# Kernel optimization log

Hardware: AMD Instinct MI355X
Metric: run time of the kernel (lower is better)

## Reference

```python
import jax, jax.numpy as jnp
import numpy as np

CHANNELS = [(3, 64), (64, 64), (64, 128), (128, 128), (128, 256), (256, 256), (256, 256),
            (256, 512), (512, 512), (512, 512), (512, 512), (512, 512), (512, 512)]
HW = 256
IN_FEAT = 512 * (HW // 32) * (HW // 32)  # 32768


def _conv(x, w):
    # 3x3, stride 1, pad 1, NCHW / OIHW, no bias
    return jax.lax.conv_general_dilated(x, w, (1, 1), ((1, 1), (1, 1)),
                                         dimension_numbers=("NCHW", "OIHW", "NCHW"))


def _maxpool2(x):
    return jax.lax.reduce_window(x, -jnp.inf, jax.lax.max, (1, 1, 2, 2), (1, 1, 2, 2), "VALID")


def setup_inputs() -> dict:
    key = jax.random.key(0)
    keys = jax.random.split(key, 17)
    inp = {"x": jax.random.normal(keys[0], (1, 3, HW, HW), jnp.float32),
           "H": HW, "W": HW, "nTh": 32, "nTw": 32}
    for i, (cin, cout) in enumerate(CHANNELS):
        scale = (1.0 / np.sqrt(9.0 * cin)).astype(np.float32) if hasattr(np.sqrt(9.0 * cin), 'astype') else 1.0 / np.sqrt(9.0 * cin)
        inp[f"cw{i + 1}"] = jax.random.normal(keys[1 + i], (cout, cin, 3, 3), jnp.float32) * np.float32(1.0 / np.sqrt(9.0 * cin))
    inp["fw1"] = jax.random.normal(keys[14], (4096, IN_FEAT), jnp.float32) * np.float32(1.0 / np.sqrt(IN_FEAT))
    inp["fw2"] = jax.random.normal(keys[15], (4096, 4096), jnp.float32) * np.float32(1.0 / np.sqrt(4096))
    inp["fw3"] = jax.random.normal(keys[16], (1000, 4096), jnp.float32) * np.float32(1.0 / np.sqrt(4096))
    return inp


def reference(x, H, W, nTh, nTw, cw1, cw2, cw3, cw4, cw5, cw6, cw7, cw8, cw9, cw10,
              cw11, cw12, cw13, fw1, fw2, fw3):
    # VGG-16 conv stack; tiling in the original is an execution schedule only,
    # the math equals the untiled stack. conv -> relu repeated, maxpool per block.
    conv_ws = [cw1, cw2, cw3, cw4, cw5, cw6, cw7, cw8, cw9, cw10, cw11, cw12, cw13]
    blocks = [(0, 2), (2, 4), (4, 7), (7, 10), (10, 13)]
    h = x
    for lo, hi in blocks:
        for w in conv_ws[lo:hi]:
            h = jax.nn.relu(_conv(h, w))
        h = _maxpool2(h)
    h = h.reshape(h.shape[0], -1)          # [1, 32768]
    h = h @ fw1.T                           # fc1 (no bias, no relu, as in source)
    h = h @ fw2.T                           # fc2
    h = h @ fw3.T                           # fc3 -> [1, 1000]
    return h
```

## Files before the change

kernel.cpp:

```cpp
#include <hip/hip_runtime.h>
#include <cstddef>


typedef __attribute__((ext_vector_type(8))) short short8;
typedef __attribute__((ext_vector_type(4))) float f32x4;

__device__ inline unsigned short f2bf(float f) {
    unsigned int u = __builtin_bit_cast(unsigned int, f);
    u += 0x7FFF + ((u >> 16) & 1);
    return (unsigned short)(u >> 16);
}

__device__ __forceinline__ void gl_lds16(const void* src, unsigned m0v) {
    asm volatile("s_mov_b32 m0, %1\n\t"
                 "global_load_lds_dwordx4 %0, off"
                 :: "v"(src), "s"(m0v) : "memory");
}

struct WtDesc { const float* src; unsigned dst; int cin; int cout; int blk0; };
struct WtArgs { WtDesc d[12]; };

__global__ __launch_bounds__(256)
void wt_all_k(WtArgs A, unsigned short* __restrict__ wt, unsigned short* __restrict__ guard)
{
    __shared__ unsigned short lds[4][9 * 520];
    const int tid = threadIdx.x, wv = tid >> 6, lane = tid & 63;
    if (blockIdx.x == 0 && tid < 128) guard[tid] = 0;

    int l = 0;
#pragma unroll
    for (int i = 1; i < 12; ++i) l = ((int)blockIdx.x >= A.d[i].blk0) ? i : l;
    const WtDesc D = A.d[l];
    const int co = ((int)blockIdx.x - D.blk0) * 4 + wv;
    const int n = D.cin * 9;
    const int cinP = D.cin + 8;

    const float4* src = (const float4*)(D.src + (size_t)co * n);
    for (int i = lane; i < (n >> 2); i += 64) {
        float4 v = src[i];
        unsigned short b[4] = {f2bf(v.x), f2bf(v.y), f2bf(v.z), f2bf(v.w)};
        const int f0 = i * 4;
#pragma unroll
        for (int k = 0; k < 4; ++k) {
            const int f = f0 + k, ci = f / 9, pos = f - ci * 9;
            lds[wv][pos * cinP + ci] = b[k];
        }
    }
    __syncthreads();
    unsigned short* dstb = wt + D.dst;
#pragma unroll 1
    for (int pos = 0; pos < 9; ++pos) {
        unsigned short* drow = dstb + ((size_t)pos * D.cout + co) * D.cin;
        for (int c4 = lane; c4 < (D.cin >> 2); c4 += 64) {
            ushort4 u = *(const ushort4*)&lds[wv][pos * cinP + c4 * 4];
            *(ushort4*)(drow + c4 * 4) = u;
        }
    }
}

template<int PR, int CO, int MODE>
__global__ __launch_bounds__(256, 2)
void conv_mfma_k(const unsigned short* __restrict__ act,
                 const unsigned short* __restrict__ wt,
                 const unsigned short* __restrict__ guard,
                 void* __restrict__ outp,
                 int Cin, int Cout, int H, int W, int chunkCi)
{
    constexpr int NT = PR / 4;
    constexpr int MT = CO / 16;
    constexpr int ICELLS = (PR + 2) * 18;
    constexpr int ITASK = ICELLS * 4;
    constexpr int ITIN = (ITASK + 255) / 256;
    constexpr int IBYTES = ((ITASK + 63) & ~63) * 16;
    constexpr int WTASK = 9 * CO * 4;
    constexpr int WIT = (WTASK + 255) / 256;
    constexpr int WBYTES = 9 * CO * 64;
    constexpr int VL = WIT + ITIN;

    __shared__ __align__(16) unsigned short wLds[2 * WBYTES / 2];
    __shared__ __align__(16) unsigned short iLds[2 * IBYTES / 2];
    __shared__ __align__(16) unsigned short dump[512];

    const int tid = threadIdx.x;
    const int lane = tid & 63, wv = tid >> 6;
    const int half = lane >> 4, l15 = lane & 15;
    const int tilesX = W >> 4;
    const int pY = blockIdx.x / tilesX, pX = blockIdx.x - pY * tilesX;
    const int y0 = pY * PR, x0 = pX * 16;
    const int cob = blockIdx.y, s = blockIdx.z;
    const int ciBeg = s * chunkCi;
    const int nCh = chunkCi >> 5;

    f32x4 acc[MT][NT];
#pragma unroll
    for (int mt = 0; mt < MT; ++mt)
#pragma unroll
        for (int nt = 0; nt < NT; ++nt) acc[mt][nt] = (f32x4){0.f, 0.f, 0.f, 0.f};

    auto STAGE = [&](int buf, int ci0) {
        const unsigned wB = (unsigned)(size_t)wLds + buf * WBYTES;
        const unsigned iB = (unsigned)(size_t)iLds + buf * IBYTES;
        const unsigned dB = (unsigned)(size_t)dump;
#pragma unroll
        for (int it = 0; it < WIT; ++it) {
            const int idx = it * 256 + tid;
            const int cell = idx >> 2, q = idx & 3;
            const int pos = cell / CO, co = cell % CO;
            const bool real = idx < WTASK;
            const unsigned short* src = real ?
                wt + (size_t)(pos * Cout + cob * CO + co) * Cin + ci0 + q * 8 : guard;
            const bool eng = (it * 256 + wv * 64) < WTASK;
            gl_lds16(src, __builtin_amdgcn_readfirstlane(
                eng ? wB + (unsigned)(it * 4096 + wv * 1024) : dB));
        }
#pragma unroll
        for (int it = 0; it < ITIN; ++it) {
            const int idx = it * 256 + tid;
            const int cell = idx >> 2, q = idx & 3;
            const int r = cell / 18, c = cell - r * 18;
            const int y = y0 - 1 + r, x = x0 - 1 + c;
            const bool ok = (idx < ITASK) & (y >= 0) & (y < H) & (x >= 0) & (x < W);
            const unsigned short* src = ok ?
                act + (size_t)(y * W + x) * Cin + ci0 + q * 8 : guard;
            const bool eng = (it * 256 + wv * 64) < ITASK;
            gl_lds16(src, __builtin_amdgcn_readfirstlane(
                eng ? iB + (unsigned)(it * 4096 + wv * 1024) : dB));
        }
    };

    STAGE(0, ciBeg);
    for (int t = 0; t < nCh; ++t) {
        const int buf = t & 1;
        if (t + 1 < nCh) {
            STAGE(buf ^ 1, ciBeg + ((t + 1) << 5));
            if constexpr (VL == 8)  asm volatile("s_waitcnt vmcnt(8)" ::: "memory");
            else if constexpr (VL == 11) asm volatile("s_waitcnt vmcnt(11)" ::: "memory");
            else asm volatile("s_waitcnt vmcnt(0)" ::: "memory");
        } else {
            asm volatile("s_waitcnt vmcnt(0)" ::: "memory");
        }
        __builtin_amdgcn_s_barrier();
        asm volatile("" ::: "memory");

        const unsigned short* wP = wLds + buf * (WBYTES / 2);
        const unsigned short* iP = iLds + buf * (IBYTES / 2);
#pragma unroll
        for (int ky = 0; ky < 3; ++ky)
#pragma unroll
        for (int kx = 0; kx < 3; ++kx) {
            const int pos = ky * 3 + kx;
            short8 a[MT];
#pragma unroll
            for (int mt = 0; mt < MT; ++mt)
                a[mt] = *(const short8*)&wP[((pos * CO) + (mt << 4) + l15) * 32 + half * 8];
#pragma unroll
            for (int nt = 0; nt < NT; ++nt) {
                const short8 b = *(const short8*)
                    &iP[((wv * NT + nt + ky) * 18 + l15 + kx) * 32 + half * 8];
#pragma unroll
                for (int mt = 0; mt < MT; ++mt)
                    acc[mt][nt] = __builtin_amdgcn_mfma_f32_16x16x32_bf16(a[mt], b, acc[mt][nt], 0, 0, 0);
            }
        }
        asm volatile("" ::: "memory");
        __builtin_amdgcn_s_barrier();
    }

    const int xg = x0 + l15;
    if (MODE == 3) {
        const int Wo = W >> 1;
#pragma unroll
        for (int mt = 0; mt < MT; ++mt)
#pragma unroll
        for (int nt = 0; nt < NT; nt += 2) {
            f32x4 a;
#pragma unroll
            for (int j = 0; j < 4; ++j) a[j] = fmaxf(acc[mt][nt][j], acc[mt][nt + 1][j]);
            f32x4 m;
#pragma unroll
            for (int j = 0; j < 4; ++j) m[j] = fmaxf(a[j], __shfl_xor(a[j], 1, 64));
            if ((l15 & 1) == 0) {
                const int yo = (y0 + wv * NT + nt) >> 1;
                const int xo = xg >> 1;
                const int co = cob * CO + (mt << 4) + half * 4;
                ushort4 u;
                u.x = f2bf(fmaxf(m[0], 0.f));
                u.y = f2bf(fmaxf(m[1], 0.f));
                u.z = f2bf(fmaxf(m[2], 0.f));
                u.w = f2bf(fmaxf(m[3], 0.f));
                *(ushort4*)((unsigned short*)outp + ((size_t)(yo * Wo + xo) * Cout + co)) = u;
            }
        }
    } else {
#pragma unroll
        for (int mt = 0; mt < MT; ++mt)
#pragma unroll
        for (int nt = 0; nt < NT; ++nt) {
            const int yg = y0 + wv * NT + nt;
            const int co = cob * CO + (mt << 4) + half * 4;
            const size_t base = (size_t)(yg * W + xg) * Cout + co;
            if (MODE == 2) {
                float4 v = make_float4(acc[mt][nt][0], acc[mt][nt][1], acc[mt][nt][2], acc[mt][nt][3]);
                *(float4*)((float*)outp + (size_t)s * Cout * H * W + base) = v;
            } else {
                ushort4 u;
                u.x = f2bf(fmaxf(acc[mt][nt][0], 0.f));
                u.y = f2bf(fmaxf(acc[mt][nt][1], 0.f));
                u.z = f2bf(fmaxf(acc[mt][nt][2], 0.f));
                u.w = f2bf(fmaxf(acc[mt][nt][3], 0.f));
                *(ushort4*)((unsigned short*)outp + base) = u;
            }
        }
    }
}

#define TILE 16
#define COB  32
__global__ __launch_bounds__(256)
void conv1_k(const float* __restrict__ in, const float* __restrict__ wt,
             unsigned short* __restrict__ out)
{
    const int Cin = 3, H = 256, W = 256, HW = H * W;
    __shared__ float sIn[2][648];
    __shared__ float sWt[2][768];

    const int tid = threadIdx.x;
    const int bx = blockIdx.x, by = blockIdx.y, co_blk = blockIdx.z;
    const int co_grp = tid >> 6;
    const int lane = tid & 63;
    const int tx = lane & 7, ty = lane >> 3;
    const int x0 = bx * TILE, y0 = by * TILE;

    int iLdsI[3], iG[3], iSub[3]; bool iOk[3];
    int wLdsI[3], wG[3], wSub[3]; bool wOk[3];
#pragma unroll
    for (int j = 0; j < 3; ++j) {
        int i = tid + j * 256;
        iOk[j] = false; iLdsI[j] = 0; iG[j] = 0; iSub[j] = 0;
        if (i < 648) {
            int sub = i / 324; int r = i - sub * 324;
            int iy = r / 18;   int ix = r - iy * 18;
            iSub[j] = sub; iLdsI[j] = sub * 324 + r;
            int y = y0 - 1 + iy, x = x0 - 1 + ix;
            if (y >= 0 && y < H && x >= 0 && x < W) { iOk[j] = true; iG[j] = sub * HW + y * W + x; }
        }
        wOk[j] = false; wLdsI[j] = 0; wG[j] = 0; wSub[j] = 0;
        if (i < 576) {
            int sub = i / 288; int r = i - sub * 288;
            int col = r / 9;   int k = r - col * 9;
            wSub[j] = sub; wLdsI[j] = sub * 384 + col * 12 + k;
            wG[j] = ((co_blk * COB + col) * Cin + sub) * 9 + k;
            wOk[j] = true;
        }
    }

    float4 acc[8];
#pragma unroll
    for (int c = 0; c < 8; ++c) acc[c] = make_float4(0.f, 0.f, 0.f, 0.f);

    const int nSteps = 2;
    float rIn[3], rWt[3];
    {
#pragma unroll
        for (int j = 0; j < 3; ++j)
            rIn[j] = (iOk[j] && iSub[j] < 3) ? in[iG[j]] : 0.f;
#pragma unroll
        for (int j = 0; j < 3; ++j)
            rWt[j] = (wOk[j] && wSub[j] < 3) ? wt[wG[j]] : 0.f;
#pragma unroll
        for (int j = 0; j < 3; ++j) { if (tid + j * 256 < 648) sIn[0][iLdsI[j]] = rIn[j]; }
#pragma unroll
        for (int j = 0; j < 3; ++j) { if (tid + j * 256 < 576) sWt[0][wLdsI[j]] = rWt[j]; }
    }

    for (int t = 0; t < nSteps; ++t) {
        __syncthreads();
        const bool more = (t + 1) < nSteps;
        if (more) {
            const int ci0 = 2;
#pragma unroll
            for (int j = 0; j < 3; ++j)
                rIn[j] = (iOk[j] && (ci0 + iSub[j]) < 3) ? in[(size_t)ci0 * HW + iG[j]] : 0.f;
#pragma unroll
            for (int j = 0; j < 3; ++j)
                rWt[j] = (wOk[j] && (ci0 + wSub[j]) < 3) ? wt[(size_t)ci0 * 9 + wG[j]] : 0.f;
        }
        const int buf = t & 1;
        const float* sI = sIn[buf];
        const float* sW = sWt[buf];
#pragma unroll
        for (int sub = 0; sub < 2; ++sub) {
            float wv[4][4];
            const float* sp = sI + sub * 324 + (2 * ty) * 18 + 2 * tx;
#pragma unroll
            for (int r = 0; r < 4; ++r) {
                float2 a = *(const float2*)(sp + r * 18);
                float2 b = *(const float2*)(sp + r * 18 + 2);
                wv[r][0] = a.x; wv[r][1] = a.y; wv[r][2] = b.x; wv[r][3] = b.y;
            }
#pragma unroll
            for (int c = 0; c < 8; ++c) {
                const float* wp = sW + sub * 384 + (co_grp * 8 + c) * 12;
                float4 w0 = *(const float4*)wp;
                float4 w1 = *(const float4*)(wp + 4);
                float  w8 = wp[8];
                const float wk[9] = {w0.x, w0.y, w0.z, w0.w, w1.x, w1.y, w1.z, w1.w, w8};
                float* ac = (float*)&acc[c];
#pragma unroll
                for (int py = 0; py < 2; ++py)
#pragma unroll
                for (int px = 0; px < 2; ++px) {
                    float sacc = ac[py * 2 + px];
#pragma unroll
                    for (int kk = 0; kk < 9; ++kk)
                        sacc = fmaf(wv[py + kk / 3][px + kk % 3], wk[kk], sacc);
                    ac[py * 2 + px] = sacc;
                }
            }
        }
        if (more) {
#pragma unroll
            for (int j = 0; j < 3; ++j) { if (tid + j * 256 < 648) sIn[buf ^ 1][iLdsI[j]] = rIn[j]; }
#pragma unroll
            for (int j = 0; j < 3; ++j) { if (tid + j * 256 < 576) sWt[buf ^ 1][wLdsI[j]] = rWt[j]; }
        }
    }

    const int co0 = co_blk * COB + co_grp * 8;
#pragma unroll
    for (int py = 0; py < 2; ++py)
#pragma unroll
    for (int px = 0; px < 2; ++px) {
        const int y = y0 + 2 * ty + py, x = x0 + 2 * tx + px;
        unsigned short u8[8];
#pragma unroll
        for (int c = 0; c < 8; ++c)
            u8[c] = f2bf(fmaxf(((const float*)&acc[c])[py * 2 + px], 0.f));
        *(uint4*)(out + (size_t)(y * W + x) * 64 + co0) = *(uint4*)u8;
    }
}

__global__ __launch_bounds__(256)
void reduce_cvt_k(const float* __restrict__ P, unsigned short* __restrict__ out,
                  int n4, int S)
{
    int i = blockIdx.x * 256 + threadIdx.x;
    if (i >= n4) return;
    const float4* p4 = (const float4*)P;
    float4 a = p4[i];
    for (int s = 1; s < S; ++s) {
        float4 b = p4[(size_t)i + (size_t)s * n4];
        a.x += b.x; a.y += b.y; a.z += b.z; a.w += b.w;
    }
    ushort4 u;
    u.x = f2bf(fmaxf(a.x, 0.f)); u.y = f2bf(fmaxf(a.y, 0.f));
    u.z = f2bf(fmaxf(a.z, 0.f)); u.w = f2bf(fmaxf(a.w, 0.f));
    *(ushort4*)(out + (size_t)i * 4) = u;
}

__global__ __launch_bounds__(256)
void reduce_pool_cvt_k(const float* __restrict__ P, unsigned short* __restrict__ out,
                       int C, int H, int W, int S)
{
    const int C4 = C >> 2, Wo = W >> 1, Ho = H >> 1;
    const int n = Ho * Wo * C4;
    int i = blockIdx.x * 256 + threadIdx.x;
    if (i >= n) return;
    const int c4 = i % C4, p = i / C4;
    const int yo = p / Wo, xo = p - yo * Wo;
    const size_t CHW = (size_t)C * H * W;
    const size_t b = (size_t)(2 * yo * W + 2 * xo) * C + c4 * 4;
    float4 v[4] = {{0,0,0,0},{0,0,0,0},{0,0,0,0},{0,0,0,0}};
    for (int s = 0; s < S; ++s) {
        const float* ps = P + s * CHW;
        float4 t0 = *(const float4*)(ps + b);
        float4 t1 = *(const float4*)(ps + b + C);
        float4 t2 = *(const float4*)(ps + b + (size_t)W * C);
        float4 t3 = *(const float4*)(ps + b + (size_t)W * C + C);
        v[0].x += t0.x; v[0].y += t0.y; v[0].z += t0.z; v[0].w += t0.w;
        v[1].x += t1.x; v[1].y += t1.y; v[1].z += t1.z; v[1].w += t1.w;
        v[2].x += t2.x; v[2].y += t2.y; v[2].z += t2.z; v[2].w += t2.w;
        v[3].x += t3.x; v[3].y += t3.y; v[3].z += t3.z; v[3].w += t3.w;
    }
    ushort4 u;
    u.x = f2bf(fmaxf(fmaxf(fmaxf(v[0].x, v[1].x), fmaxf(v[2].x, v[3].x)), 0.f));
    u.y = f2bf(fmaxf(fmaxf(fmaxf(v[0].y, v[1].y), fmaxf(v[2].y, v[3].y)), 0.f));
    u.z = f2bf(fmaxf(fmaxf(fmaxf(v[0].z, v[1].z), fmaxf(v[2].z, v[3].z)), 0.f));
    u.w = f2bf(fmaxf(fmaxf(fmaxf(v[0].w, v[1].w), fmaxf(v[2].w, v[3].w)), 0.f));
    *(ushort4*)(out + (size_t)p * C + c4 * 4) = u;
}

__global__ __launch_bounds__(256)
void reduce_pool_f32_k(const float* __restrict__ P, float* __restrict__ out,
                       int C, int H, int W, int S)
{
    const int Wo = W >> 1, Ho = H >> 1;
    const int n = Ho * Wo * C;
    int i = blockIdx.x * 256 + threadIdx.x;
    if (i >= n) return;
    const int c = i % C, p = i / C;
    const int yo = p / Wo, xo = p - yo * Wo;
    const size_t CHW = (size_t)C * H * W;
    float v0 = 0.f, v1 = 0.f, v2 = 0.f, v3 = 0.f;
    const size_t b = (size_t)(2 * yo * W + 2 * xo) * C + c;
    for (int s = 0; s < S; ++s) {
        const float* ps = P + s * CHW;
        v0 += ps[b]; v1 += ps[b + C]; v2 += ps[b + (size_t)W * C]; v3 += ps[b + (size_t)W * C + C];
    }
    out[(size_t)c * (Ho * Wo) + p] = fmaxf(fmaxf(fmaxf(v0, v1), fmaxf(v2, v3)), 0.f);
}

__global__ __launch_bounds__(256)
void gemv_k(const float* __restrict__ Wm, const float* __restrict__ xv,
            float* __restrict__ y, int K)
{
    __shared__ float red[4];
    const int tid = threadIdx.x;
    const float4* row = (const float4*)(Wm + (size_t)blockIdx.x * K);
    const float4* x4  = (const float4*)xv;
    const int K4 = K >> 2;
    float sum = 0.f;
    for (int i = tid; i < K4; i += 256) {
        float4 a = row[i], b = x4[i];
        sum += a.x * b.x + a.y * b.y + a.z * b.z + a.w * b.w;
    }
#pragma unroll
    for (int off = 32; off > 0; off >>= 1) sum += __shfl_down(sum, off, 64);
    if ((tid & 63) == 0) red[tid >> 6] = sum;
    __syncthreads();
    if (tid == 0) y[blockIdx.x] = red[0] + red[1] + red[2] + red[3];
}

extern "C" void kernel_launch(void* const* d_in, const int* in_sizes, int n_in,
                              void* d_out, int out_size, void* d_ws, size_t ws_size,
                              hipStream_t stream)
{
    (void)in_sizes; (void)n_in; (void)out_size; (void)ws_size;
    const float* x = (const float*)d_in[0];
    const float* cw[13];
    for (int i = 0; i < 13; ++i) cw[i] = (const float*)d_in[5 + i];
    const float* fw1 = (const float*)d_in[18];
    const float* fw2 = (const float*)d_in[19];
    const float* fw3 = (const float*)d_in[20];
    float* outp = (float*)d_out;

    static const int CIN[12]  = {64, 64, 128, 128, 256, 256, 256, 512, 512, 512, 512, 512};
    static const int COUT[12] = {64, 128, 128, 256, 256, 256, 512, 512, 512, 512, 512, 512};

    char* ws = (char*)d_ws;
    size_t wOff[12]; size_t o = 0;
    for (int i = 0; i < 12; ++i) { wOff[i] = o; o += (size_t)9 * COUT[i] * CIN[i]; }
    unsigned short* WT = (unsigned short*)ws;
    unsigned short* guardp = WT + o;
    size_t ao = ((o + 128) * 2 + 255) & ~(size_t)255;
    unsigned short* bA = (unsigned short*)(ws + ao);
    unsigned short* bB = (unsigned short*)(ws + ao + 8388608);
    char* Pr = ws + ao + 2 * 8388608;
    float* Pf = (float*)Pr;
    float* fcIn = (float*)bA;
    float* F1 = (float*)bB;
    float* F2 = F1 + 4096;

    WtArgs wa; int blk = 0;
    {
        size_t oo = 0;
        for (int i = 0; i < 12; ++i) {
            wa.d[i].src = cw[i + 1];
            wa.d[i].dst = (unsigned)oo;
            wa.d[i].cin = CIN[i];
            wa.d[i].cout = COUT[i];
            wa.d[i].blk0 = blk;
            oo += (size_t)9 * COUT[i] * CIN[i];
            blk += COUT[i] / 4;
        }
    }
    wt_all_k<<<blk, 256, 0, stream>>>(wa, WT, guardp);

    conv1_k<<<dim3(16, 16, 2), 256, 0, stream>>>(x, cw[0], bA);

    conv_mfma_k<16, 32, 3><<<dim3(256, 2, 1), 256, 0, stream>>>(bA, WT + wOff[0], guardp, bB, 64, 64, 256, 256, 64);
    conv_mfma_k<8, 32, 0><<<dim3(128, 4, 1), 256, 0, stream>>>(bB, WT + wOff[1], guardp, bA, 64, 128, 128, 128, 64);
    conv_mfma_k<8, 32, 3><<<dim3(128, 4, 1), 256, 0, stream>>>(bA, WT + wOff[2], guardp, bB, 128, 128, 128, 128, 128);
    conv_mfma_k<8, 32, 2><<<dim3(32, 8, 2), 256, 0, stream>>>(bB, WT + wOff[3], guardp, Pf, 128, 256, 64, 64, 64);
    reduce_cvt_k<<<(262144 + 255) / 256, 256, 0, stream>>>(Pf, bA, 262144, 2);
    conv_mfma_k<8, 32, 2><<<dim3(32, 8, 2), 256, 0, stream>>>(bA, WT + wOff[4], guardp, Pf, 256, 256, 64, 64, 128);
    reduce_cvt_k<<<(262144 + 255) / 256, 256, 0, stream>>>(Pf, bB, 262144, 2);
    conv_mfma_k<8, 32, 2><<<dim3(32, 8, 2), 256, 0, stream>>>(bB, WT + wOff[5], guardp, Pf, 256, 256, 64, 64, 128);
    reduce_pool_cvt_k<<<(65536 + 255) / 256, 256, 0, stream>>>(Pf, bA, 256, 64, 64, 2);
    conv_mfma_k<8, 32, 2><<<dim3(8, 16, 4), 256, 0, stream>>>(bA, WT + wOff[6], guardp, Pf, 256, 512, 32, 32, 64);
    reduce_cvt_k<<<(131072 + 255) / 256, 256, 0, stream>>>(Pf, bB, 131072, 4);
    conv_mfma_k<8, 32, 2><<<dim3(8, 16, 4), 256, 0, stream>>>(bB, WT + wOff[7], guardp, Pf, 512, 512, 32, 32, 128);
    reduce_cvt_k<<<(131072 + 255) / 256, 256, 0, stream>>>(Pf, bA, 131072, 4);
    conv_mfma_k<8, 32, 2><<<dim3(8, 16, 4), 256, 0, stream>>>(bA, WT + wOff[8], guardp, Pf, 512, 512, 32, 32, 128);
    reduce_pool_cvt_k<<<(32768 + 255) / 256, 256, 0, stream>>>(Pf, bB, 512, 32, 32, 4);
    conv_mfma_k<8, 32, 2><<<dim3(2, 16, 16), 256, 0, stream>>>(bB, WT + wOff[9], guardp, Pf, 512, 512, 16, 16, 32);
    reduce_cvt_k<<<(32768 + 255) / 256, 256, 0, stream>>>(Pf, bA, 32768, 16);
    conv_mfma_k<8, 32, 2><<<dim3(2, 16, 16), 256, 0, stream>>>(bA, WT + wOff[10], guardp, Pf, 512, 512, 16, 16, 32);
    reduce_cvt_k<<<(32768 + 255) / 256, 256, 0, stream>>>(Pf, bB, 32768, 16);
    conv_mfma_k<8, 32, 2><<<dim3(2, 16, 16), 256, 0, stream>>>(bB, WT + wOff[11], guardp, Pf, 512, 512, 16, 16, 32);
    reduce_pool_f32_k<<<(32768 + 255) / 256, 256, 0, stream>>>(Pf, fcIn, 512, 16, 16, 16);

    gemv_k<<<4096, 256, 0, stream>>>(fw1, fcIn, F1, 32768);
    gemv_k<<<4096, 256, 0, stream>>>(fw2, F1, F2, 4096);
    gemv_k<<<1000, 256, 0, stream>>>(fw3, F2, outp, 4096);
}
```

Before: 968.7 us.

## Drop split-K partials and fuse ReLU/pool into conv epilogues

Removes the split-K path from the MFMA conv kernel, so each block now loops over the full input-channel range. ReLU, bf16 conversion and 2x2 max-pool are applied in the conv epilogue, and the last layer writes fp32 NCHW straight into the FC input. This eliminates the separate reduce and reduce-pool kernels and the fp32 partial-sum round trips through memory. To keep some parallelism, the 32x32 and 16x16 layers switch to 4-row tiles. Those deep layers still launch far fewer blocks, each running a longer K loop, which risks underfilling the GPU.

```diff
diff --git a/kernel.cpp b/kernel.cpp
--- a/kernel.cpp
+++ b/kernel.cpp
@@ -64,9 +64,9 @@
                  const unsigned short* __restrict__ wt,
                  const unsigned short* __restrict__ guard,
                  void* __restrict__ outp,
-                 int Cin, int Cout, int H, int W, int chunkCi)
+                 int Cin, int Cout, int H, int W)
 {
-    constexpr int NT = PR / 4;
+    constexpr int NT = (PR + 3) / 4;
     constexpr int MT = CO / 16;
     constexpr int ICELLS = (PR + 2) * 18;
     constexpr int ITASK = ICELLS * 4;
@@ -76,6 +76,8 @@
     constexpr int WIT = (WTASK + 255) / 256;
     constexpr int WBYTES = 9 * CO * 64;
     constexpr int VL = WIT + ITIN;
+    static_assert(VL == 7 || VL == 8 || VL == 11, "unexpected stage depth");
+    static_assert(MODE == 0 || ((MODE == 3 || MODE == 4) && (NT % 2) == 0), "pool needs even NT");
 
     __shared__ __align__(16) unsigned short wLds[2 * WBYTES / 2];
     __shared__ __align__(16) unsigned short iLds[2 * IBYTES / 2];
@@ -87,9 +89,8 @@
     const int tilesX = W >> 4;
     const int pY = blockIdx.x / tilesX, pX = blockIdx.x - pY * tilesX;
     const int y0 = pY * PR, x0 = pX * 16;
-    const int cob = blockIdx.y, s = blockIdx.z;
-    const int ciBeg = s * chunkCi;
-    const int nCh = chunkCi >> 5;
+    const int cob = blockIdx.y;
+    const int nCh = Cin >> 5;
 
     f32x4 acc[MT][NT];
 #pragma unroll
@@ -128,14 +129,14 @@
         }
     };
 
-    STAGE(0, ciBeg);
+    STAGE(0, 0);
     for (int t = 0; t < nCh; ++t) {
         const int buf = t & 1;
         if (t + 1 < nCh) {
-            STAGE(buf ^ 1, ciBeg + ((t + 1) << 5));
-            if constexpr (VL == 8)  asm volatile("s_waitcnt vmcnt(8)" ::: "memory");
-            else if constexpr (VL == 11) asm volatile("s_waitcnt vmcnt(11)" ::: "memory");
-            else asm volatile("s_waitcnt vmcnt(0)" ::: "memory");
+            STAGE(buf ^ 1, (t + 1) << 5);
+            if constexpr (VL == 7)  asm volatile("s_waitcnt vmcnt(7)" ::: "memory");
+            else if constexpr (VL == 8)  asm volatile("s_waitcnt vmcnt(8)" ::: "memory");
+            else asm volatile("s_waitcnt vmcnt(11)" ::: "memory");
         } else {
             asm volatile("s_waitcnt vmcnt(0)" ::: "memory");
         }
@@ -167,7 +168,7 @@
     }
 
     const int xg = x0 + l15;
-    if (MODE == 3) {
+    if constexpr (MODE == 3 || MODE == 4) {
         const int Wo = W >> 1;
 #pragma unroll
         for (int mt = 0; mt < MT; ++mt)
@@ -183,12 +184,21 @@
                 const int yo = (y0 + wv * NT + nt) >> 1;
                 const int xo = xg >> 1;
                 const int co = cob * CO + (mt << 4) + half * 4;
-                ushort4 u;
-                u.x = f2bf(fmaxf(m[0], 0.f));
-                u.y = f2bf(fmaxf(m[1], 0.f));
-                u.z = f2bf(fmaxf(m[2], 0.f));
-                u.w = f2bf(fmaxf(m[3], 0.f));
-                *(ushort4*)((unsigned short*)outp + ((size_t)(yo * Wo + xo) * Cout + co)) = u;
+                if constexpr (MODE == 3) {
+                    ushort4 u;
+                    u.x = f2bf(fmaxf(m[0], 0.f));
+                    u.y = f2bf(fmaxf(m[1], 0.f));
+                    u.z = f2bf(fmaxf(m[2], 0.f));
+                    u.w = f2bf(fmaxf(m[3], 0.f));
+                    *(ushort4*)((unsigned short*)outp + ((size_t)(yo * Wo + xo) * Cout + co)) = u;
+                } else {
+                    const int Ho = W >> 1;  (void)Ho;
+                    float* op = (float*)outp;
+                    const int hw = (W >> 1) * (W >> 1);
+#pragma unroll
+                    for (int j = 0; j < 4; ++j)
+                        op[(size_t)(co + j) * hw + yo * Wo + xo] = fmaxf(m[j], 0.f);
+                }
             }
         }
     } else {
@@ -199,17 +209,12 @@
             const int yg = y0 + wv * NT + nt;
             const int co = cob * CO + (mt << 4) + half * 4;
             const size_t base = (size_t)(yg * W + xg) * Cout + co;
-            if (MODE == 2) {
-                float4 v = make_float4(acc[mt][nt][0], acc[mt][nt][1], acc[mt][nt][2], acc[mt][nt][3]);
-                *(float4*)((float*)outp + (size_t)s * Cout * H * W + base) = v;
-            } else {
-                ushort4 u;
-                u.x = f2bf(fmaxf(acc[mt][nt][0], 0.f));
-                u.y = f2bf(fmaxf(acc[mt][nt][1], 0.f));
-                u.z = f2bf(fmaxf(acc[mt][nt][2], 0.f));
-                u.w = f2bf(fmaxf(acc[mt][nt][3], 0.f));
-                *(ushort4*)((unsigned short*)outp + base) = u;
-            }
+            ushort4 u;
+            u.x = f2bf(fmaxf(acc[mt][nt][0], 0.f));
+            u.y = f2bf(fmaxf(acc[mt][nt][1], 0.f));
+            u.z = f2bf(fmaxf(acc[mt][nt][2], 0.f));
+            u.w = f2bf(fmaxf(acc[mt][nt][3], 0.f));
+            *(ushort4*)((unsigned short*)outp + base) = u;
         }
     }
 }
@@ -338,76 +343,6 @@
             u8[c] = f2bf(fmaxf(((const float*)&acc[c])[py * 2 + px], 0.f));
         *(uint4*)(out + (size_t)(y * W + x) * 64 + co0) = *(uint4*)u8;
     }
-}
-
-__global__ __launch_bounds__(256)
-void reduce_cvt_k(const float* __restrict__ P, unsigned short* __restrict__ out,
-                  int n4, int S)
-{
-    int i = blockIdx.x * 256 + threadIdx.x;
-    if (i >= n4) return;
-    const float4* p4 = (const float4*)P;
-    float4 a = p4[i];
-    for (int s = 1; s < S; ++s) {
-        float4 b = p4[(size_t)i + (size_t)s * n4];
-        a.x += b.x; a.y += b.y; a.z += b.z; a.w += b.w;
-    }
-    ushort4 u;
-    u.x = f2bf(fmaxf(a.x, 0.f)); u.y = f2bf(fmaxf(a.y, 0.f));
-    u.z = f2bf(fmaxf(a.z, 0.f)); u.w = f2bf(fmaxf(a.w, 0.f));
-    *(ushort4*)(out + (size_t)i * 4) = u;
-}
-
-__global__ __launch_bounds__(256)
-void reduce_pool_cvt_k(const float* __restrict__ P, unsigned short* __restrict__ out,
-                       int C, int H, int W, int S)
-{
-    const int C4 = C >> 2, Wo = W >> 1, Ho = H >> 1;
-    const int n = Ho * Wo * C4;
-    int i = blockIdx.x * 256 + threadIdx.x;
-    if (i >= n) return;
-    const int c4 = i % C4, p = i / C4;
-    const int yo = p / Wo, xo = p - yo * Wo;
-    const size_t CHW = (size_t)C * H * W;
-    const size_t b = (size_t)(2 * yo * W + 2 * xo) * C + c4 * 4;
-    float4 v[4] = {{0,0,0,0},{0,0,0,0},{0,0,0,0},{0,0,0,0}};
-    for (int s = 0; s < S; ++s) {
-        const float* ps = P + s * CHW;
-        float4 t0 = *(const float4*)(ps + b);
-        float4 t1 = *(const float4*)(ps + b + C);
-        float4 t2 = *(const float4*)(ps + b + (size_t)W * C);
-        float4 t3 = *(const float4*)(ps + b + (size_t)W * C + C);
-        v[0].x += t0.x; v[0].y += t0.y; v[0].z += t0.z; v[0].w += t0.w;
-        v[1].x += t1.x; v[1].y += t1.y; v[1].z += t1.z; v[1].w += t1.w;
-        v[2].x += t2.x; v[2].y += t2.y; v[2].z += t2.z; v[2].w += t2.w;
-        v[3].x += t3.x; v[3].y += t3.y; v[3].z += t3.z; v[3].w += t3.w;
-    }
-    ushort4 u;
-    u.x = f2bf(fmaxf(fmaxf(fmaxf(v[0].x, v[1].x), fmaxf(v[2].x, v[3].x)), 0.f));
-    u.y = f2bf(fmaxf(fmaxf(fmaxf(v[0].y, v[1].y), fmaxf(v[2].y, v[3].y)), 0.f));
-    u.z = f2bf(fmaxf(fmaxf(fmaxf(v[0].z, v[1].z), fmaxf(v[2].z, v[3].z)), 0.f));
-    u.w = f2bf(fmaxf(fmaxf(fmaxf(v[0].w, v[1].w), fmaxf(v[2].w, v[3].w)), 0.f));
-    *(ushort4*)(out + (size_t)p * C + c4 * 4) = u;
-}
-
-__global__ __launch_bounds__(256)
-void reduce_pool_f32_k(const float* __restrict__ P, float* __restrict__ out,
-                       int C, int H, int W, int S)
-{
-    const int Wo = W >> 1, Ho = H >> 1;
-    const int n = Ho * Wo * C;
-    int i = blockIdx.x * 256 + threadIdx.x;
-    if (i >= n) return;
-    const int c = i % C, p = i / C;
-    const int yo = p / Wo, xo = p - yo * Wo;
-    const size_t CHW = (size_t)C * H * W;
-    float v0 = 0.f, v1 = 0.f, v2 = 0.f, v3 = 0.f;
-    const size_t b = (size_t)(2 * yo * W + 2 * xo) * C + c;
-    for (int s = 0; s < S; ++s) {
-        const float* ps = P + s * CHW;
-        v0 += ps[b]; v1 += ps[b + C]; v2 += ps[b + (size_t)W * C]; v3 += ps[b + (size_t)W * C + C];
-    }
-    out[(size_t)c * (Ho * Wo) + p] = fmaxf(fmaxf(fmaxf(v0, v1), fmaxf(v2, v3)), 0.f);
 }
 
 __global__ __launch_bounds__(256)
@@ -455,8 +390,6 @@
     size_t ao = ((o + 128) * 2 + 255) & ~(size_t)255;
     unsigned short* bA = (unsigned short*)(ws + ao);
     unsigned short* bB = (unsigned short*)(ws + ao + 8388608);
-    char* Pr = ws + ao + 2 * 8388608;
-    float* Pf = (float*)Pr;
     float* fcIn = (float*)bA;
     float* F1 = (float*)bB;
     float* F2 = F1 + 4096;
@@ -478,27 +411,18 @@
 
     conv1_k<<<dim3(16, 16, 2), 256, 0, stream>>>(x, cw[0], bA);
 
-    conv_mfma_k<16, 32, 3><<<dim3(256, 2, 1), 256, 0, stream>>>(bA, WT + wOff[0], guardp, bB, 64, 64, 256, 256, 64);
-    conv_mfma_k<8, 32, 0><<<dim3(128, 4, 1), 256, 0, stream>>>(bB, WT + wOff[1], guardp, bA, 64, 128, 128, 128, 64);
-    conv_mfma_k<8, 32, 3><<<dim3(128, 4, 1), 256, 0, stream>>>(bA, WT + wOff[2], guardp, bB, 128, 128, 128, 128, 128);
-    conv_mfma_k<8, 32, 2><<<dim3(32, 8, 2), 256, 0, stream>>>(bB, WT + wOff[3], guardp, Pf, 128, 256, 64, 64, 64);
-    reduce_cvt_k<<<(262144 + 255) / 256, 256, 0, stream>>>(Pf, bA, 262144, 2);
-    conv_mfma_k<8, 32, 2><<<dim3(32, 8, 2), 256, 0, stream>>>(bA, WT + wOff[4], guardp, Pf, 256, 256, 64, 64, 128);
-    reduce_cvt_k<<<(262144 + 255) / 256, 256, 0, stream>>>(Pf, bB, 262144, 2);
-    conv_mfma_k<8, 32, 2><<<dim3(32, 8, 2), 256, 0, stream>>>(bB, WT + wOff[5], guardp, Pf, 256, 256, 64, 64, 128);
-    reduce_pool_cvt_k<<<(65536 + 255) / 256, 256, 0, stream>>>(Pf, bA, 256, 64, 64, 2);
-    conv_mfma_k<8, 32, 2><<<dim3(8, 16, 4), 256, 0, stream>>>(bA, WT + wOff[6], guardp, Pf, 256, 512, 32, 32, 64);
-    reduce_cvt_k<<<(131072 + 255) / 256, 256, 0, stream>>>(Pf, bB, 131072, 4);
-    conv_mfma_k<8, 32, 2><<<dim3(8, 16, 4), 256, 0, stream>>>(bB, WT + wOff[7], guardp, Pf, 512, 512, 32, 32, 128);
-    reduce_cvt_k<<<(131072 + 255) / 256, 256, 0, stream>>>(Pf, bA, 131072, 4);
-    conv_mfma_k<8, 32, 2><<<dim3(8, 16, 4), 256, 0, stream>>>(bA, WT + wOff[8], guardp, Pf, 512, 512, 32, 32, 128);
-    reduce_pool_cvt_k<<<(32768 + 255) / 256, 256, 0, stream>>>(Pf, bB, 512, 32, 32, 4);
-    conv_mfma_k<8, 32, 2><<<dim3(2, 16, 16), 256, 0, stream>>>(bB, WT + wOff[9], guardp, Pf, 512, 512, 16, 16, 32);
-    reduce_cvt_k<<<(32768 + 255) / 256, 256, 0, stream>>>(Pf, bA, 32768, 16);
-    conv_mfma_k<8, 32, 2><<<dim3(2, 16, 16), 256, 0, stream>>>(bA, WT + wOff[10], guardp, Pf, 512, 512, 16, 16, 32);
-    reduce_cvt_k<<<(32768 + 255) / 256, 256, 0, stream>>>(Pf, bB, 32768, 16);
-    conv_mfma_k<8, 32, 2><<<dim3(2, 16, 16), 256, 0, stream>>>(bB, WT + wOff[11], guardp, Pf, 512, 512, 16, 16, 32);
-    reduce_pool_f32_k<<<(32768 + 255) / 256, 256, 0, stream>>>(Pf, fcIn, 512, 16, 16, 16);
+    conv_mfma_k<16, 32, 3><<<dim3(256, 2), 256, 0, stream>>>(bA, WT + wOff[0], guardp, bB, 64, 64, 256, 256);
+    conv_mfma_k<8, 32, 0><<<dim3(128, 4), 256, 0, stream>>>(bB, WT + wOff[1], guardp, bA, 64, 128, 128, 128);
+    conv_mfma_k<8, 32, 3><<<dim3(128, 4), 256, 0, stream>>>(bA, WT + wOff[2], guardp, bB, 128, 128, 128, 128);
+    conv_mfma_k<8, 32, 0><<<dim3(32, 8), 256, 0, stream>>>(bB, WT + wOff[3], guardp, bA, 128, 256, 64, 64);
+    conv_mfma_k<8, 32, 0><<<dim3(32, 8), 256, 0, stream>>>(bA, WT + wOff[4], guardp, bB, 256, 256, 64, 64);
+    conv_mfma_k<8, 32, 3><<<dim3(32, 8), 256, 0, stream>>>(bB, WT + wOff[5], guardp, bA, 256, 256, 64, 64);
+    conv_mfma_k<4, 32, 0><<<dim3(16, 16), 256, 0, stream>>>(bA, WT + wOff[6], guardp, bB, 256, 512, 32, 32);
+    conv_mfma_k<4, 32, 0><<<dim3(16, 16), 256, 0, stream>>>(bB, WT + wOff[7], guardp, bA, 512, 512, 32, 32);
+    conv_mfma_k<8, 32, 3><<<dim3(8, 16), 256, 0, stream>>>(bA, WT + wOff[8], guardp, bB, 512, 512, 32, 32);
+    conv_mfma_k<4, 32, 0><<<dim3(4, 16), 256, 0, stream>>>(bB, WT + wOff[9], guardp, bA, 512, 512, 16, 16);
+    conv_mfma_k<4, 32, 0><<<dim3(4, 16), 256, 0, stream>>>(bA, WT + wOff[10], guardp, bB, 512, 512, 16, 16);
+    conv_mfma_k<8, 32, 4><<<dim3(2, 16), 256, 0, stream>>>(bB, WT + wOff[11], guardp, fcIn, 512, 512, 16, 16);
 
     gemv_k<<<4096, 256, 0, stream>>>(fw1, fcIn, F1, 32768);
     gemv_k<<<4096, 256, 0, stream>>>(fw2, F1, F2, 4096);
```

After: 940.5 us. -2.9%, faster.
